# Kernel optimization log

Measured on AMD Instinct MI355X. Metric: run time of the kernel, lower is better.

The kernel has to match this reference:

```python
import jax, jax.numpy as jnp
import numpy as np

TEMPERATURE = 0.1
NEG_INF = -1e30  # finite sentinel to keep logsumexp grad-safe


def setup_inputs() -> dict:
    key = jax.random.key(0)
    k_emb, k_lab = jax.random.split(key)
    B, D, C = 8192, 256, 100
    embeddings = jax.random.normal(k_emb, (B, D), dtype=jnp.float32)
    labels = jax.random.randint(k_lab, (B,), 0, C, dtype=jnp.int64)
    return {"embeddings": embeddings, "labels": labels}


def reference(embeddings, labels):
    B = embeddings.shape[0]
    # squared L2 pairwise distance: ||x_i||^2 + ||x_j||^2 - 2 x_i . x_j
    sq = jnp.sum(embeddings * embeddings, axis=1)  # [B]
    gram = jnp.einsum('id,jd->ij', embeddings, embeddings)  # [B,B]
    dist2 = jnp.maximum(sq[:, None] + sq[None, :] - 2.0 * gram, 0.0)
    sim = -dist2 / TEMPERATURE  # [B,B]

    same = labels[:, None] == labels[None, :]
    eye = jnp.eye(B, dtype=bool)
    pos_mask = same & ~eye
    neg_mask = ~same

    # per-row uniform random positive via Gumbel-argmax over pos_mask
    k_sel = jax.random.key(42)
    g = jax.random.gumbel(k_sel, (B, B), dtype=jnp.float32)
    j = jnp.argmax(jnp.where(pos_mask, g, -jnp.inf), axis=1)  # [B]

    numerator = jnp.take_along_axis(sim, j[:, None], axis=1)[:, 0]  # sim[i, j_i]
    denominator = jax.nn.logsumexp(jnp.where(neg_mask, sim, NEG_INF), axis=1)

    valid = pos_mask.any(axis=1) & neg_mask.any(axis=1)
    per_row = -(numerator - denominator)
    n_valid = jnp.sum(valid)
    loss = jnp.sum(jnp.where(valid, per_row, 0.0)) / jnp.maximum(n_valid, 1)
    return jnp.where(n_valid > 0, loss, 0.0)
```

## Files before the change

### kernel.cpp

```cpp
#include <hip/hip_runtime.h>
#include <float.h>
#include <math.h>


#define B_N 8192
#define D_K 256
#define NCLS 100
#define MAXC 512
#define NSPLIT 16
#define NPART NSPLIT
#define JR (B_N / NSPLIT)
#define BI 64
#define BJ 128
#define NJT (JR / BJ)
#define BK 64
#define NKC (D_K / BK)
#define NEG_INF -1e30f
#define C2F  (-14.426950408889634f)
#define K2A  (28.853900817779268f)
#define LN2F (0.6931471805599453f)

typedef __attribute__((ext_vector_type(8))) short bf16x8;
typedef __attribute__((ext_vector_type(4))) float f32x4;
typedef unsigned short ushort_t;

__device__ __forceinline__ float ex2(float x){ return __builtin_amdgcn_exp2f(x); }
__device__ __forceinline__ float lg2(float x){ return __builtin_amdgcn_logf(x); }

__device__ __forceinline__ unsigned rotl32(unsigned x, int d){ return (x << d) | (x >> (32 - d)); }

__device__ __forceinline__ float gumbel_at(unsigned idx){
  const unsigned HALF = (unsigned)B_N * (unsigned)B_N / 2u;
  unsigned c0, c1; bool second;
  if (idx < HALF){ c0 = idx; c1 = idx + HALF; second = false; }
  else            { c0 = idx - HALF; c1 = idx; second = true; }
  const unsigned ks0 = 0u, ks1 = 42u, ks2 = 0u ^ 42u ^ 0x1BD11BDAu;
  unsigned x0 = c0 + ks0, x1 = c1 + ks1;
#define TF_RND(r) { x0 += x1; x1 = rotl32(x1, (r)); x1 ^= x0; }
  TF_RND(13) TF_RND(15) TF_RND(26) TF_RND(6)   x0 += ks1; x1 += ks2 + 1u;
  TF_RND(17) TF_RND(29) TF_RND(16) TF_RND(24)  x0 += ks2; x1 += ks0 + 2u;
  TF_RND(13) TF_RND(15) TF_RND(26) TF_RND(6)   x0 += ks0; x1 += ks1 + 3u;
  TF_RND(17) TF_RND(29) TF_RND(16) TF_RND(24)  x0 += ks1; x1 += ks2 + 4u;
  TF_RND(13) TF_RND(15) TF_RND(26) TF_RND(6)   x0 += ks2; x1 += ks0 + 5u;
#undef TF_RND
  unsigned bits = second ? x1 : x0;
  float u = __uint_as_float((bits >> 9) | 0x3f800000u) - 1.0f;
  const float TINY = 1.17549435e-38f;
  u = u * (1.0f - TINY) + TINY;
  u = fmaxf(TINY, u);
  return -logf(-logf(u));
}

__device__ __forceinline__ ushort_t f2bf(float x){
  unsigned u = __float_as_uint(x);
  return (ushort_t)((u + 0x7FFFu + ((u >> 16) & 1u)) >> 16);
}

__device__ __forceinline__ void async16(const ushort_t* g, ushort_t* lds_wave_base){
  __builtin_amdgcn_global_load_lds((const __attribute__((address_space(1))) void*)g,
                                   (__attribute__((address_space(3))) void*)lds_wave_base,
                                   16, 0, 0);
}

__global__ __launch_bounds__(256)
void prep_kernel(const float* __restrict__ E, ushort_t* __restrict__ Ebf,
                 float* __restrict__ sq, float* __restrict__ acc4,
                 const int* __restrict__ labels, int* __restrict__ cls_cnt,
                 int* __restrict__ clist){
  __shared__ int s_list[MAXC];
  __shared__ int s_n;
  if (blockIdx.x < B_N / 4){
    if (blockIdx.x == 0 && threadIdx.x < 4) acc4[threadIdx.x] = 0.f;
    int w = threadIdx.x >> 6, lane = threadIdx.x & 63;
    int row = blockIdx.x * 4 + w;
    const float4 v = *reinterpret_cast<const float4*>(E + (size_t)row * D_K + lane * 4);
    float s = v.x*v.x + v.y*v.y + v.z*v.z + v.w*v.w;
#pragma unroll
    for (int off = 32; off > 0; off >>= 1) s += __shfl_down(s, off);
    if (lane == 0) sq[row] = s;
    ushort4 o; o.x = f2bf(v.x); o.y = f2bf(v.y); o.z = f2bf(v.z); o.w = f2bf(v.w);
    *reinterpret_cast<ushort4*>(Ebf + (size_t)row * D_K + lane * 4) = o;
  } else {
    const int c = blockIdx.x - B_N / 4;
    const int tid = threadIdx.x;
    if (tid == 0) s_n = 0;
    __syncthreads();
    for (int t = tid; t < B_N; t += 256){
      if (labels[t] == c){
        int p = atomicAdd(&s_n, 1);
        if (p < MAXC) s_list[p] = t;
      }
    }
    __syncthreads();
    const int n = min(s_n, MAXC);
    if (tid == 0) cls_cnt[c] = n;
    for (int t = tid; t < n; t += 256) clist[c * MAXC + t] = s_list[t];
  }
}

__global__ __launch_bounds__(256)
void rowsel_kernel(const int* __restrict__ labels, const int* __restrict__ cls_cnt,
                   const int* __restrict__ clist, int* __restrict__ jsel){
  const int w = threadIdx.x >> 6, lane = threadIdx.x & 63;
  const int row = blockIdx.x * 4 + w;
  const int c = labels[row];
  const int n = min(cls_cnt[c], MAXC);
  float gb = -FLT_MAX; int jb = -1;
  for (int t = lane; t < n; t += 64){
    int j = clist[c * MAXC + t];
    if (j != row){
      float g = gumbel_at(((unsigned)row << 13) + (unsigned)j);
      if (g > gb || (g == gb && (unsigned)j < (unsigned)jb)){ gb = g; jb = j; }
    }
  }
#pragma unroll
  for (int off = 32; off > 0; off >>= 1){
    float g2 = __shfl_down(gb, off);
    int   j2 = __shfl_down(jb, off);
    if (g2 > gb || (g2 == gb && (unsigned)j2 < (unsigned)jb)){ gb = g2; jb = j2; }
  }
  if (lane == 0) jsel[row] = jb;
}

__global__ __launch_bounds__(256, 4)
void fused_kernel(const ushort_t* __restrict__ Ebf, const int* __restrict__ labels,
                  const float* __restrict__ sq, const int* __restrict__ jsel,
                  float* __restrict__ numer,
                  float* __restrict__ wsM, float* __restrict__ wsS)
{
  __shared__ __align__(16) ushort_t Bs[2][BJ * BK];
  __shared__ float s_h2j[JR];
  __shared__ int   s_lj[JR];
  __shared__ float s_h2i[BI];
  __shared__ int   s_li[BI];
  __shared__ int   s_ji[BI];

  const int bi    = blockIdx.x >> 4;
  const int split = blockIdx.x & 15;
  const int i0    = bi * BI;
  const int jbase = split * JR;
  const int tid   = threadIdx.x;
  const int lane  = tid & 63;
  const int w     = tid >> 6;
  const int quad  = lane >> 4;
  const int l15   = lane & 15;

  for (int t = tid; t < JR; t += 256){ s_h2j[t] = C2F * sq[jbase + t]; s_lj[t] = labels[jbase + t]; }
  if (tid < BI){ s_h2i[tid] = C2F * sq[i0 + tid]; s_li[tid] = labels[i0 + tid]; s_ji[tid] = jsel[i0 + tid]; }

  bf16x8 af[8];
  {
    const ushort_t* rp = Ebf + (size_t)(i0 + w * 16 + l15) * D_K + quad * 8;
#pragma unroll
    for (int c = 0; c < 8; c++)
      af[c] = *reinterpret_cast<const bf16x8*>(rp + c * 32);
  }

  f32x4 acc[8];
#pragma unroll
  for (int nt = 0; nt < 8; nt++) acc[nt] = (f32x4)0.f;
  float sm[4], ssum[4];
#pragma unroll
  for (int r = 0; r < 4; r++){ sm[r] = NEG_INF; ssum[r] = 0.f; }

  int soff[4];
#pragma unroll
  for (int rd = 0; rd < 4; rd++){
    int slot = rd * 256 + tid;
    int r = slot >> 3, gs = slot & 7;
    soff[rd] = r * D_K + ((gs ^ (r & 7)) << 3);
  }

#pragma unroll
  for (int rd = 0; rd < 4; rd++)
    async16(Ebf + (size_t)jbase * D_K + soff[rd],
            &Bs[0][(size_t)(rd * 256 + w * 64) * 8]);
  __syncthreads();

#pragma unroll 1
  for (int jt = 0; jt < NJT; jt++){
    const int j0 = jbase + jt * BJ;
#pragma unroll
    for (int kc = 0; kc < NKC; kc++){
      const int b = kc & 1;
      const int sn = jt * NKC + kc + 1;
      if (sn < NJT * NKC){
        const int kcn = sn & 3;
        const size_t gb0 = (size_t)(jbase + (sn >> 2) * BJ) * D_K + (size_t)kcn * BK;
#pragma unroll
        for (int rd = 0; rd < 4; rd++)
          async16(Ebf + gb0 + soff[rd],
                  &Bs[b ^ 1][(size_t)(rd * 256 + w * 64) * 8]);
      }
#pragma unroll
      for (int s = 0; s < 2; s++){
        const int g = s * 4 + quad;
        const int c = kc * 2 + s;
#pragma unroll
        for (int h = 0; h < 2; h++){
          bf16x8 bfr[4];
#pragma unroll
          for (int q = 0; q < 4; q++){
            int r = (h * 4 + q) * 16 + l15;
            bfr[q] = *reinterpret_cast<const bf16x8*>(&Bs[b][r * BK + ((g ^ (r & 7)) << 3)]);
          }
#pragma unroll
          for (int q = 0; q < 4; q++)
            acc[h * 4 + q] = __builtin_amdgcn_mfma_f32_16x16x32_bf16(af[c], bfr[q], acc[h * 4 + q], 0, 0, 0);
        }
      }
      if (kc == NKC - 1){
        float h2j[8]; int lj[8];
#pragma unroll
        for (int nt = 0; nt < 8; nt++){
          int ccol = jt * BJ + nt * 16 + l15;
          h2j[nt] = s_h2j[ccol]; lj[nt] = s_lj[ccol];
        }
#pragma unroll
        for (int rr = 0; rr < 4; rr++){
          const int rl = w * 16 + quad * 4 + rr;
          const float h2i = s_h2i[rl];
          const int lrow = s_li[rl], jsl = s_ji[rl];
          float sv[8];
#pragma unroll
          for (int nt = 0; nt < 8; nt++){
            float a = acc[nt][rr];
            float sim2 = fminf(fmaf(K2A, a, h2i + h2j[nt]), 0.f);
            int colg = j0 + nt * 16 + l15;
            if (colg == jsl) numer[i0 + rl] = sim2;
            sv[nt] = (lj[nt] != lrow) ? sim2 : NEG_INF;
          }
          float m8 = fmaxf(fmaxf(fmaxf(sv[0],sv[1]),fmaxf(sv[2],sv[3])),
                           fmaxf(fmaxf(sv[4],sv[5]),fmaxf(sv[6],sv[7])));
          float s8 = ex2(sv[0]-m8)+ex2(sv[1]-m8)+ex2(sv[2]-m8)+ex2(sv[3]-m8)
                   + ex2(sv[4]-m8)+ex2(sv[5]-m8)+ex2(sv[6]-m8)+ex2(sv[7]-m8);
          float M = fmaxf(sm[rr], m8);
          ssum[rr] = ssum[rr]*ex2(sm[rr]-M) + s8*ex2(m8-M);
          sm[rr] = M;
        }
#pragma unroll
        for (int nt = 0; nt < 8; nt++) acc[nt] = (f32x4)0.f;
      }
      __syncthreads();
    }
  }

#pragma unroll
  for (int rr = 0; rr < 4; rr++){
    float mv = sm[rr], sv2 = ssum[rr];
#pragma unroll
    for (int mask = 1; mask < 16; mask <<= 1){
      float m2 = __shfl_xor(mv, mask);
      float s2 = __shfl_xor(sv2, mask);
      float M = fmaxf(mv, m2);
      sv2 = sv2 * ex2(mv - M) + s2 * ex2(m2 - M);
      mv = M;
    }
    if (l15 == 0){
      int rl = w * 16 + quad * 4 + rr;
      int o = split * B_N + i0 + rl;
      wsM[o] = mv; wsS[o] = sv2;
    }
  }
}

__global__ __launch_bounds__(256)
void finale_kernel(const float* __restrict__ wsM, const float* __restrict__ wsS,
                   const float* __restrict__ numer, const int* __restrict__ jsel,
                   float* __restrict__ acc4, float* __restrict__ out)
{
  const int tid = threadIdx.x;
  const int row = blockIdx.x * 256 + tid;
  float M = -3.0e38f, S = 0.f;
#pragma unroll
  for (int p = 0; p < NPART; p++){
    float m2 = wsM[p * B_N + row], s2 = wsS[p * B_N + row];
    float Mn = fmaxf(M, m2);
    S = S * ex2(M - Mn) + s2 * ex2(m2 - Mn);
    M = Mn;
  }
  bool v = (jsel[row] >= 0) && (M > -5e29f);
  float s = v ? (LN2F * (M + lg2(S) - numer[row])) : 0.f;
  unsigned n = v ? 1u : 0u;
#pragma unroll
  for (int off = 32; off > 0; off >>= 1){ s += __shfl_down(s, off); n += __shfl_down(n, off); }
  __shared__ float ssm[4]; __shared__ unsigned snm[4];
  if ((tid & 63) == 0){ ssm[tid >> 6] = s; snm[tid >> 6] = n; }
  __syncthreads();
  if (tid == 0){
    float bs = ssm[0] + ssm[1] + ssm[2] + ssm[3];
    unsigned bn = snm[0] + snm[1] + snm[2] + snm[3];
    atomicAdd(&acc4[0], bs);
    atomicAdd((unsigned*)&acc4[1], bn);
    __threadfence();
    unsigned old = atomicAdd((unsigned*)&acc4[2], 1u);
    if (old == 31u){
      float St = atomicAdd(&acc4[0], 0.f);
      unsigned Nt = atomicAdd((unsigned*)&acc4[1], 0u);
      out[0] = (Nt > 0u) ? (St / (float)Nt) : 0.f;
    }
  }
}

extern "C" void kernel_launch(void* const* d_in, const int* in_sizes, int n_in,
                              void* d_out, int out_size, void* d_ws, size_t ws_size,
                              hipStream_t stream)
{
  const float* E      = (const float*)d_in[0];
  const int*   labels = (const int*)d_in[1];
  float*       out    = (float*)d_out;

  ushort_t* Ebf = (ushort_t*)d_ws;
  float* wsM    = (float*)(Ebf + (size_t)B_N * D_K);
  float* wsS    = wsM + NPART * B_N;
  float* sqb    = wsS + NPART * B_N;
  float* numer  = sqb + B_N;
  int* jsel     = (int*)(numer + B_N);
  float* acc4   = (float*)(jsel + B_N);
  int* cls_cnt  = (int*)(acc4 + 4);
  int* clist    = cls_cnt + NCLS;

  prep_kernel<<<B_N / 4 + NCLS, 256, 0, stream>>>(E, Ebf, sqb, acc4, labels, cls_cnt, clist);
  rowsel_kernel<<<B_N / 4, 256, 0, stream>>>(labels, cls_cnt, clist, jsel);
  fused_kernel<<<(B_N / BI) * NSPLIT, 256, 0, stream>>>(Ebf, labels, sqb, jsel, numer, wsM, wsS);
  finale_kernel<<<B_N / 256, 256, 0, stream>>>(wsM, wsS, numer, jsel, acc4, out);
}
```

Baseline: 133.6 us.

## Reshape fused tile to 128 rows by 64 columns with two M-tiles per wave

The fused distance/logsumexp kernel now gives each wave 32 rows (two 16-row MFMA tiles) against 64 columns, instead of 16 rows against 128 columns. Each B fragment read from LDS now feeds two MFMAs, which halves LDS traffic per MFMA, and the B staging buffer shrinks. The cost is twice as many A-fragment registers, a lower occupancy hint (3 blocks instead of 4), half as many blocks, and online-softmax merges over 4 columns instead of 8, which means more rescale exponentials.

```diff
diff --git a/kernel.cpp b/kernel.cpp
--- a/kernel.cpp
+++ b/kernel.cpp
@@ -10,8 +10,8 @@
 #define NSPLIT 16
 #define NPART NSPLIT
 #define JR (B_N / NSPLIT)
-#define BI 64
-#define BJ 128
+#define BI 128
+#define BJ 64
 #define NJT (JR / BJ)
 #define BK 64
 #define NKC (D_K / BK)
@@ -122,7 +122,7 @@
   if (lane == 0) jsel[row] = jb;
 }
 
-__global__ __launch_bounds__(256, 4)
+__global__ __launch_bounds__(256, 3)
 void fused_kernel(const ushort_t* __restrict__ Ebf, const int* __restrict__ labels,
                   const float* __restrict__ sq, const int* __restrict__ jsel,
                   float* __restrict__ numer,
@@ -148,31 +148,34 @@
   for (int t = tid; t < JR; t += 256){ s_h2j[t] = C2F * sq[jbase + t]; s_lj[t] = labels[jbase + t]; }
   if (tid < BI){ s_h2i[tid] = C2F * sq[i0 + tid]; s_li[tid] = labels[i0 + tid]; s_ji[tid] = jsel[i0 + tid]; }
 
-  bf16x8 af[8];
-  {
-    const ushort_t* rp = Ebf + (size_t)(i0 + w * 16 + l15) * D_K + quad * 8;
+  bf16x8 af[2][8];
+#pragma unroll
+  for (int mt = 0; mt < 2; mt++){
+    const ushort_t* rp = Ebf + (size_t)(i0 + w * 32 + mt * 16 + l15) * D_K + quad * 8;
 #pragma unroll
     for (int c = 0; c < 8; c++)
-      af[c] = *reinterpret_cast<const bf16x8*>(rp + c * 32);
-  }
-
-  f32x4 acc[8];
-#pragma unroll
-  for (int nt = 0; nt < 8; nt++) acc[nt] = (f32x4)0.f;
-  float sm[4], ssum[4];
-#pragma unroll
-  for (int r = 0; r < 4; r++){ sm[r] = NEG_INF; ssum[r] = 0.f; }
-
-  int soff[4];
-#pragma unroll
-  for (int rd = 0; rd < 4; rd++){
+      af[mt][c] = *reinterpret_cast<const bf16x8*>(rp + c * 32);
+  }
+
+  f32x4 acc[2][4];
+#pragma unroll
+  for (int mt = 0; mt < 2; mt++)
+#pragma unroll
+    for (int nt = 0; nt < 4; nt++) acc[mt][nt] = (f32x4)0.f;
+  float sm[8], ssum[8];
+#pragma unroll
+  for (int r = 0; r < 8; r++){ sm[r] = NEG_INF; ssum[r] = 0.f; }
+
+  int soff[2];
+#pragma unroll
+  for (int rd = 0; rd < 2; rd++){
     int slot = rd * 256 + tid;
     int r = slot >> 3, gs = slot & 7;
     soff[rd] = r * D_K + ((gs ^ (r & 7)) << 3);
   }
 
 #pragma unroll
-  for (int rd = 0; rd < 4; rd++)
+  for (int rd = 0; rd < 2; rd++)
     async16(Ebf + (size_t)jbase * D_K + soff[rd],
             &Bs[0][(size_t)(rd * 256 + w * 64) * 8]);
   __syncthreads();
@@ -188,7 +191,7 @@
         const int kcn = sn & 3;
         const size_t gb0 = (size_t)(jbase + (sn >> 2) * BJ) * D_K + (size_t)kcn * BK;
 #pragma unroll
-        for (int rd = 0; rd < 4; rd++)
+        for (int rd = 0; rd < 2; rd++)
           async16(Ebf + gb0 + soff[rd],
                   &Bs[b ^ 1][(size_t)(rd * 256 + w * 64) * 8]);
       }
@@ -196,58 +199,61 @@
       for (int s = 0; s < 2; s++){
         const int g = s * 4 + quad;
         const int c = kc * 2 + s;
-#pragma unroll
-        for (int h = 0; h < 2; h++){
-          bf16x8 bfr[4];
-#pragma unroll
-          for (int q = 0; q < 4; q++){
-            int r = (h * 4 + q) * 16 + l15;
-            bfr[q] = *reinterpret_cast<const bf16x8*>(&Bs[b][r * BK + ((g ^ (r & 7)) << 3)]);
-          }
-#pragma unroll
-          for (int q = 0; q < 4; q++)
-            acc[h * 4 + q] = __builtin_amdgcn_mfma_f32_16x16x32_bf16(af[c], bfr[q], acc[h * 4 + q], 0, 0, 0);
+        bf16x8 bfr[4];
+#pragma unroll
+        for (int q = 0; q < 4; q++){
+          int r = q * 16 + l15;
+          bfr[q] = *reinterpret_cast<const bf16x8*>(&Bs[b][r * BK + ((g ^ (r & 7)) << 3)]);
+        }
+#pragma unroll
+        for (int q = 0; q < 4; q++){
+          acc[0][q] = __builtin_amdgcn_mfma_f32_16x16x32_bf16(af[0][c], bfr[q], acc[0][q], 0, 0, 0);
+          acc[1][q] = __builtin_amdgcn_mfma_f32_16x16x32_bf16(af[1][c], bfr[q], acc[1][q], 0, 0, 0);
         }
       }
       if (kc == NKC - 1){
-        float h2j[8]; int lj[8];
-#pragma unroll
-        for (int nt = 0; nt < 8; nt++){
+        float h2j[4]; int lj[4];
+#pragma unroll
+        for (int nt = 0; nt < 4; nt++){
           int ccol = jt * BJ + nt * 16 + l15;
           h2j[nt] = s_h2j[ccol]; lj[nt] = s_lj[ccol];
         }
 #pragma unroll
-        for (int rr = 0; rr < 4; rr++){
-          const int rl = w * 16 + quad * 4 + rr;
-          const float h2i = s_h2i[rl];
-          const int lrow = s_li[rl], jsl = s_ji[rl];
-          float sv[8];
-#pragma unroll
-          for (int nt = 0; nt < 8; nt++){
-            float a = acc[nt][rr];
-            float sim2 = fminf(fmaf(K2A, a, h2i + h2j[nt]), 0.f);
-            int colg = j0 + nt * 16 + l15;
-            if (colg == jsl) numer[i0 + rl] = sim2;
-            sv[nt] = (lj[nt] != lrow) ? sim2 : NEG_INF;
+        for (int mt = 0; mt < 2; mt++){
+#pragma unroll
+          for (int rr = 0; rr < 4; rr++){
+            const int rl = w * 32 + mt * 16 + quad * 4 + rr;
+            const float h2i = s_h2i[rl];
+            const int lrow = s_li[rl], jsl = s_ji[rl];
+            float sv[4];
+#pragma unroll
+            for (int nt = 0; nt < 4; nt++){
+              float a = acc[mt][nt][rr];
+              float sim2 = fminf(fmaf(K2A, a, h2i + h2j[nt]), 0.f);
+              int colg = j0 + nt * 16 + l15;
+              if (colg == jsl) numer[i0 + rl] = sim2;
+              sv[nt] = (lj[nt] != lrow) ? sim2 : NEG_INF;
+            }
+            float m4 = fmaxf(fmaxf(sv[0], sv[1]), fmaxf(sv[2], sv[3]));
+            float s4 = ex2(sv[0]-m4)+ex2(sv[1]-m4)+ex2(sv[2]-m4)+ex2(sv[3]-m4);
+            const int sidx = mt * 4 + rr;
+            float M = fmaxf(sm[sidx], m4);
+            ssum[sidx] = ssum[sidx]*ex2(sm[sidx]-M) + s4*ex2(m4-M);
+            sm[sidx] = M;
           }
-          float m8 = fmaxf(fmaxf(fmaxf(sv[0],sv[1]),fmaxf(sv[2],sv[3])),
-                           fmaxf(fmaxf(sv[4],sv[5]),fmaxf(sv[6],sv[7])));
-          float s8 = ex2(sv[0]-m8)+ex2(sv[1]-m8)+ex2(sv[2]-m8)+ex2(sv[3]-m8)
-                   + ex2(sv[4]-m8)+ex2(sv[5]-m8)+ex2(sv[6]-m8)+ex2(sv[7]-m8);
-          float M = fmaxf(sm[rr], m8);
-          ssum[rr] = ssum[rr]*ex2(sm[rr]-M) + s8*ex2(m8-M);
-          sm[rr] = M;
         }
 #pragma unroll
-        for (int nt = 0; nt < 8; nt++) acc[nt] = (f32x4)0.f;
+        for (int mt = 0; mt < 2; mt++)
+#pragma unroll
+          for (int nt = 0; nt < 4; nt++) acc[mt][nt] = (f32x4)0.f;
       }
       __syncthreads();
     }
   }
 
 #pragma unroll
-  for (int rr = 0; rr < 4; rr++){
-    float mv = sm[rr], sv2 = ssum[rr];
+  for (int sidx = 0; sidx < 8; sidx++){
+    float mv = sm[sidx], sv2 = ssum[sidx];
 #pragma unroll
     for (int mask = 1; mask < 16; mask <<= 1){
       float m2 = __shfl_xor(mv, mask);
@@ -257,7 +263,8 @@
       mv = M;
     }
     if (l15 == 0){
-      int rl = w * 16 + quad * 4 + rr;
+      const int mt = sidx >> 2, rr = sidx & 3;
+      int rl = w * 32 + mt * 16 + quad * 4 + rr;
       int o = split * B_N + i0 + rl;
       wsM[o] = mv; wsS[o] = sv2;
     }
```

After: 145.5 us. 1.09x slower.
